# Kernel tuning notes

Measured on AMD Instinct MI355X. Metric: run time of the kernel, lower is better.

## Reference

```python
import jax, jax.numpy as jnp
import numpy as np

LR = 0.001       # ISTA step size (default in _IstaStep)
GAMMA = 0.1      # lambdav sparsity penalty (gamma init kwarg)
N_STEPS = 10     # number of unrolled ISTA iterations


def _soft_threshold(x, t):
    # _proxOp: max(x - t, 0) + min(x + t, 0)
    return jnp.maximum(x - t, 0.0) + jnp.minimum(x + t, 0.0)


def setup_inputs() -> dict:
    key = jax.random.key(0)
    k1, k2 = jax.random.split(key)
    B, I, O = 131072, 128, 256
    inputs = jax.random.normal(k1, (B, I), dtype=jnp.float32)
    # glorot_uniform for W of shape (output_dim, input_dim)
    scale = float(np.sqrt(6.0 / (O + I)))
    W = jax.random.uniform(k2, (O, I), dtype=jnp.float32, minval=-scale, maxval=scale)
    return {"inputs": inputs, "W": W}


def reference(inputs, W):
    # inputs: [B, I]; W: [O, I]; states x: [B, O]
    B = inputs.shape[0]
    O = W.shape[0]
    x0 = jnp.zeros((B, O), dtype=inputs.dtype)

    def step(x, _):
        recon = x @ W                              # [B, I], linear activation
        # analytic grad of sum((inputs - recon)^2) w.r.t. x (what T.grad computes)
        grad = 2.0 * (recon - inputs) @ W.T        # [B, O]
        new_x = _soft_threshold(x - LR * grad, LR * GAMMA)
        # theano.gradient.disconnected_grad on the new state each step
        new_x = jax.lax.stop_gradient(new_x)
        return new_x, None

    x_final, _ = jax.lax.scan(step, x0, None, length=N_STEPS)
    # return_reconstruction=True -> dot(outs, W)
    return x_final @ W
```

## Files before the change

### kernel.cpp

```cpp
#include <hip/hip_runtime.h>
#include <hip/hip_bf16.h>

typedef __attribute__((ext_vector_type(4))) float  f32x4;
typedef __attribute__((ext_vector_type(16))) float f32x16;
typedef __attribute__((ext_vector_type(8))) short  s16x8;
typedef __attribute__((ext_vector_type(4))) short  s16x4;

#define THR_  1.0e-4f
#define SC_   2.0e-3f

__device__ __forceinline__ unsigned short f2bf(float f) {
  union { __hip_bfloat16 b; unsigned short u; } cv;
  cv.b = __float2bfloat16(f);
  return cv.u;
}
__device__ __forceinline__ float sthr(float v) {
  return v - fmaxf(fminf(v, THR_), -THR_);
}
__device__ __forceinline__ float bflo(unsigned u) {
  return __builtin_bit_cast(float, u << 16);
}
__device__ __forceinline__ float bfhi(unsigned u) {
  return __builtin_bit_cast(float, u & 0xffff0000u);
}

__global__ void sc_prep(const float* __restrict__ W, unsigned short* __restrict__ ws) {
  const int b = blockIdx.x;
  const int l = threadIdx.x;
  const int r = l & 31, h = l >> 5;
  if (b < 128) {
    const int kc = b >> 3, ntg = b & 7;
    const int n = ntg * 32 + r;
    const int k0 = kc * 16 + 8 * h;
    float s[8];
    #pragma unroll
    for (int j = 0; j < 8; ++j) s[j] = 0.0f;
    for (int i = 0; i < 128; ++i) {
      const float wn = W[n * 128 + i];
      #pragma unroll
      for (int j = 0; j < 8; ++j) s[j] += W[(k0 + j) * 128 + i] * wn;
    }
    unsigned short* dst = ws + ((unsigned)b * 64u + l) * 8u;
    #pragma unroll
    for (int j = 0; j < 8; ++j) dst[j] = f2bf(-SC_ * s[j]);
  } else if (b < 192) {
    const int bb = b - 128;
    const int kc = bb >> 3, ntg = bb & 7;
    const int n = ntg * 32 + r;
    const int k0 = kc * 16 + 8 * h;
    unsigned short* dst = ws + 65536u + ((unsigned)bb * 64u + l) * 8u;
    #pragma unroll
    for (int j = 0; j < 8; ++j) dst[j] = f2bf(SC_ * W[n * 128 + k0 + j]);
  } else {
    const int bb = b - 192;
    const int kc = bb >> 2, it = bb & 3;
    const int i = it * 32 + r;
    const int n0 = kc * 16 + 8 * h;
    unsigned short* dst = ws + 98304u + ((unsigned)bb * 64u + l) * 8u;
    #pragma unroll
    for (int j = 0; j < 8; ++j) dst[j] = f2bf(W[(n0 + j) * 128 + i]);
  }
}

__global__ __launch_bounds__(256, 2) void sc_fused(
    const float* __restrict__ inp,
    const unsigned short* __restrict__ wsp,
    float* __restrict__ outp)
{
  __shared__ __align__(16) unsigned char lds[33280];

  const int tid = threadIdx.x;
  const int l = tid & 63;
  const int w = tid >> 6;
  const int h = l >> 5;
  const int r31 = l & 31;
  const long row0 = (long)blockIdx.x * 32;

  const int rB0 = r31 * 520 + h * 16;
  const int rB1 = rB0 + 16640;
  const int wB0 = r31 * 520 + h * 8 + w * 128;
  const int wB1 = wB0 + 16640;

  #pragma unroll
  for (int rep = 0; rep < 4; ++rep) {
    const int flat = rep * 256 + tid;
    const int rr = flat >> 5;
    const int c4 = flat & 31;
    const f32x4 v = *reinterpret_cast<const f32x4*>(inp + (row0 + rr) * 128 + c4 * 4);
    s16x4 p;
    p[0] = (short)f2bf(v[0]); p[1] = (short)f2bf(v[1]);
    p[2] = (short)f2bf(v[2]); p[3] = (short)f2bf(v[3]);
    *reinterpret_cast<s16x4*>(lds + 16640 + rr * 264 + c4 * 8) = p;
  }

  s16x8 gfr[32];
  #pragma unroll
  for (int kc = 0; kc < 8; ++kc)
    #pragma unroll
    for (int nt = 0; nt < 2; ++nt)
      gfr[kc * 2 + nt] = *reinterpret_cast<const s16x8*>(
          wsp + 65536u + ((unsigned)(kc * 8 + w * 2 + nt) * 64u + l) * 8u);

  __syncthreads();

  f32x16 accA[2], accB[2], creg[2];
  #pragma unroll
  for (int nt = 0; nt < 2; ++nt)
    #pragma unroll
    for (int e = 0; e < 16; ++e) { accA[nt][e] = 0.0f; accB[nt][e] = 0.0f; }

  const int ib = 16640 + r31 * 264 + h * 16;
  #pragma unroll
  for (int kc = 0; kc < 4; ++kc) {
    const s16x8 bA = *reinterpret_cast<const s16x8*>(lds + ib + kc * 32);
    const s16x8 bB = *reinterpret_cast<const s16x8*>(lds + ib + (kc + 4) * 32);
    __builtin_amdgcn_s_setprio(1);
    #pragma unroll
    for (int nt = 0; nt < 2; ++nt)
      accA[nt] = __builtin_amdgcn_mfma_f32_32x32x16_bf16(gfr[kc * 2 + nt], bA, accA[nt], 0, 0, 0);
    #pragma unroll
    for (int nt = 0; nt < 2; ++nt)
      accB[nt] = __builtin_amdgcn_mfma_f32_32x32x16_bf16(gfr[(kc + 4) * 2 + nt], bB, accB[nt], 0, 0, 0);
    __builtin_amdgcn_s_setprio(0);
  }

  #pragma unroll
  for (int nt = 0; nt < 2; ++nt)
    #pragma unroll
    for (int q = 0; q < 4; ++q) {
      float f0 = accA[nt][4 * q + 0] + accB[nt][4 * q + 0];
      float f1 = accA[nt][4 * q + 1] + accB[nt][4 * q + 1];
      float f2 = accA[nt][4 * q + 2] + accB[nt][4 * q + 2];
      float f3 = accA[nt][4 * q + 3] + accB[nt][4 * q + 3];
      creg[nt][4 * q + 0] = f0; creg[nt][4 * q + 1] = f1;
      creg[nt][4 * q + 2] = f2; creg[nt][4 * q + 3] = f3;
      f0 = sthr(f0); f1 = sthr(f1); f2 = sthr(f2); f3 = sthr(f3);
      s16x4 p;
      p[0] = (short)f2bf(f0); p[1] = (short)f2bf(f1);
      p[2] = (short)f2bf(f2); p[3] = (short)f2bf(f3);
      *reinterpret_cast<s16x4*>(lds + wB0 + nt * 64 + q * 16) = p;
      accA[nt][4 * q + 0] = f0 + creg[nt][4 * q + 0];
      accA[nt][4 * q + 1] = f1 + creg[nt][4 * q + 1];
      accA[nt][4 * q + 2] = f2 + creg[nt][4 * q + 2];
      accA[nt][4 * q + 3] = f3 + creg[nt][4 * q + 3];
      accB[nt][4 * q + 0] = 0.0f; accB[nt][4 * q + 1] = 0.0f;
      accB[nt][4 * q + 2] = 0.0f; accB[nt][4 * q + 3] = 0.0f;
    }

  #pragma unroll
  for (int kc = 0; kc < 16; ++kc)
    #pragma unroll
    for (int nt = 0; nt < 2; ++nt)
      gfr[kc * 2 + nt] = *reinterpret_cast<const s16x8*>(
          wsp + ((unsigned)(kc * 8 + w * 2 + nt) * 64u + l) * 8u);

  if (((blockIdx.x >> 11) ^ blockIdx.x) & 1) {
    __builtin_amdgcn_s_sleep(15);
    __builtin_amdgcn_s_sleep(4);
  }

  auto STEP = [&](const int rb, const int wb) {
    __syncthreads();
    #pragma unroll
    for (int kc = 0; kc < 8; ++kc) {
      const s16x8 bA = *reinterpret_cast<const s16x8*>(lds + rb + kc * 32);
      const s16x8 bB = *reinterpret_cast<const s16x8*>(lds + rb + (kc + 8) * 32);
      __builtin_amdgcn_s_setprio(1);
      #pragma unroll
      for (int nt = 0; nt < 2; ++nt)
        accA[nt] = __builtin_amdgcn_mfma_f32_32x32x16_bf16(gfr[kc * 2 + nt], bA, accA[nt], 0, 0, 0);
      #pragma unroll
      for (int nt = 0; nt < 2; ++nt)
        accB[nt] = __builtin_amdgcn_mfma_f32_32x32x16_bf16(gfr[(kc + 8) * 2 + nt], bB, accB[nt], 0, 0, 0);
      __builtin_amdgcn_s_setprio(0);
    }
    #pragma unroll
    for (int nt = 0; nt < 2; ++nt)
      #pragma unroll
      for (int q = 0; q < 4; ++q) {
        float f0 = sthr(accA[nt][4 * q + 0] + accB[nt][4 * q + 0]);
        float f1 = sthr(accA[nt][4 * q + 1] + accB[nt][4 * q + 1]);
        float f2 = sthr(accA[nt][4 * q + 2] + accB[nt][4 * q + 2]);
        float f3 = sthr(accA[nt][4 * q + 3] + accB[nt][4 * q + 3]);
        s16x4 p;
        p[0] = (short)f2bf(f0); p[1] = (short)f2bf(f1);
        p[2] = (short)f2bf(f2); p[3] = (short)f2bf(f3);
        *reinterpret_cast<s16x4*>(lds + wb + nt * 64 + q * 16) = p;
        accA[nt][4 * q + 0] = f0 + creg[nt][4 * q + 0];
        accA[nt][4 * q + 1] = f1 + creg[nt][4 * q + 1];
        accA[nt][4 * q + 2] = f2 + creg[nt][4 * q + 2];
        accA[nt][4 * q + 3] = f3 + creg[nt][4 * q + 3];
        accB[nt][4 * q + 0] = 0.0f; accB[nt][4 * q + 1] = 0.0f;
        accB[nt][4 * q + 2] = 0.0f; accB[nt][4 * q + 3] = 0.0f;
      }
  };

  #pragma unroll 1
  for (int p = 0; p < 4; ++p) {
    STEP(rB0, wB1);
    STEP(rB1, wB0);
  }
  STEP(rB0, wB1);

  __syncthreads();
  #pragma unroll
  for (int kc = 0; kc < 16; ++kc)
    gfr[kc] = *reinterpret_cast<const s16x8*>(
        wsp + 98304u + ((unsigned)(kc * 4 + w) * 64u + l) * 8u);
  f32x16 oA, oB;
  #pragma unroll
  for (int e = 0; e < 16; ++e) { oA[e] = 0.0f; oB[e] = 0.0f; }
  #pragma unroll
  for (int kc = 0; kc < 8; ++kc) {
    const s16x8 bA = *reinterpret_cast<const s16x8*>(lds + rB1 + kc * 32);
    const s16x8 bB = *reinterpret_cast<const s16x8*>(lds + rB1 + (kc + 8) * 32);
    __builtin_amdgcn_s_setprio(1);
    oA = __builtin_amdgcn_mfma_f32_32x32x16_bf16(gfr[kc], bA, oA, 0, 0, 0);
    oB = __builtin_amdgcn_mfma_f32_32x32x16_bf16(gfr[kc + 8], bB, oB, 0, 0, 0);
    __builtin_amdgcn_s_setprio(0);
  }
  const int ob = r31 * 520 + h * 16 + w * 128;
  #pragma unroll
  for (int q = 0; q < 4; ++q) {
    f32x4 p;
    p[0] = oA[4 * q + 0] + oB[4 * q + 0]; p[1] = oA[4 * q + 1] + oB[4 * q + 1];
    p[2] = oA[4 * q + 2] + oB[4 * q + 2]; p[3] = oA[4 * q + 3] + oB[4 * q + 3];
    *reinterpret_cast<f32x4*>(lds + ob + q * 32) = p;
  }
  __syncthreads();
  #pragma unroll
  for (int rep = 0; rep < 4; ++rep) {
    const int flat = rep * 256 + tid;
    const int rr = flat >> 5;
    const int c4 = flat & 31;
    const f32x4 v = *reinterpret_cast<const f32x4*>(lds + rr * 520 + c4 * 16);
    *reinterpret_cast<f32x4*>(outp + (row0 + rr) * 128 + c4 * 4) = v;
  }
}

extern "C" void kernel_launch(void* const* d_in, const int* in_sizes, int n_in,
                              void* d_out, int out_size, void* d_ws, size_t ws_size,
                              hipStream_t stream) {
  const float* inp = (const float*)d_in[0];
  const float* W   = (const float*)d_in[1];
  unsigned short* ws = (unsigned short*)d_ws;
  float* outp = (float*)d_out;
  const int B = in_sizes[0] / 128;
  sc_prep<<<256, 64, 0, stream>>>(W, ws);
  sc_fused<<<B / 32, 256, 0, stream>>>(inp, ws, outp);
}
```

Baseline: 180.6 us.

## Pack constant term as bf16, prefetch LDS operands, drop staggered sleep

The per-row constant term (creg, 32 floats) is now stored as 16 packed bf16 pairs, which cuts register pressure. The LDS B-operand loads in the step loop are software-pipelined two iterations ahead, and setprio is hoisted out of the loop. The block-parity s_sleep stagger is removed. Storing the constant term in bf16 reduces its precision, and the extra prefetch registers partly offset the savings.

```diff
diff --git a/kernel.cpp b/kernel.cpp
--- a/kernel.cpp
+++ b/kernel.cpp
@@ -103,7 +103,7 @@
 
   __syncthreads();
 
-  f32x16 accA[2], accB[2], creg[2];
+  f32x16 accA[2], accB[2];
   #pragma unroll
   for (int nt = 0; nt < 2; ++nt)
     #pragma unroll
@@ -124,25 +124,30 @@
     __builtin_amdgcn_s_setprio(0);
   }
 
+  unsigned cp[16];
   #pragma unroll
   for (int nt = 0; nt < 2; ++nt)
     #pragma unroll
+    for (int j = 0; j < 8; ++j) {
+      const float e0 = accA[nt][2 * j + 0] + accB[nt][2 * j + 0];
+      const float e1 = accA[nt][2 * j + 1] + accB[nt][2 * j + 1];
+      cp[nt * 8 + j] = (unsigned)f2bf(e0) | ((unsigned)f2bf(e1) << 16);
+    }
+  #pragma unroll
+  for (int nt = 0; nt < 2; ++nt)
+    #pragma unroll
     for (int q = 0; q < 4; ++q) {
-      float f0 = accA[nt][4 * q + 0] + accB[nt][4 * q + 0];
-      float f1 = accA[nt][4 * q + 1] + accB[nt][4 * q + 1];
-      float f2 = accA[nt][4 * q + 2] + accB[nt][4 * q + 2];
-      float f3 = accA[nt][4 * q + 3] + accB[nt][4 * q + 3];
-      creg[nt][4 * q + 0] = f0; creg[nt][4 * q + 1] = f1;
-      creg[nt][4 * q + 2] = f2; creg[nt][4 * q + 3] = f3;
-      f0 = sthr(f0); f1 = sthr(f1); f2 = sthr(f2); f3 = sthr(f3);
+      const unsigned pa = cp[nt * 8 + q * 2], pb = cp[nt * 8 + q * 2 + 1];
+      float f0 = sthr(accA[nt][4 * q + 0] + accB[nt][4 * q + 0]);
+      float f1 = sthr(accA[nt][4 * q + 1] + accB[nt][4 * q + 1]);
+      float f2 = sthr(accA[nt][4 * q + 2] + accB[nt][4 * q + 2]);
+      float f3 = sthr(accA[nt][4 * q + 3] + accB[nt][4 * q + 3]);
       s16x4 p;
       p[0] = (short)f2bf(f0); p[1] = (short)f2bf(f1);
       p[2] = (short)f2bf(f2); p[3] = (short)f2bf(f3);
       *reinterpret_cast<s16x4*>(lds + wB0 + nt * 64 + q * 16) = p;
-      accA[nt][4 * q + 0] = f0 + creg[nt][4 * q + 0];
-      accA[nt][4 * q + 1] = f1 + creg[nt][4 * q + 1];
-      accA[nt][4 * q + 2] = f2 + creg[nt][4 * q + 2];
-      accA[nt][4 * q + 3] = f3 + creg[nt][4 * q + 3];
+      accA[nt][4 * q + 0] = f0 + bflo(pa); accA[nt][4 * q + 1] = f1 + bfhi(pa);
+      accA[nt][4 * q + 2] = f2 + bflo(pb); accA[nt][4 * q + 3] = f3 + bfhi(pb);
       accB[nt][4 * q + 0] = 0.0f; accB[nt][4 * q + 1] = 0.0f;
       accB[nt][4 * q + 2] = 0.0f; accB[nt][4 * q + 3] = 0.0f;
     }
@@ -154,30 +159,32 @@
       gfr[kc * 2 + nt] = *reinterpret_cast<const s16x8*>(
           wsp + ((unsigned)(kc * 8 + w * 2 + nt) * 64u + l) * 8u);
 
-  if (((blockIdx.x >> 11) ^ blockIdx.x) & 1) {
-    __builtin_amdgcn_s_sleep(15);
-    __builtin_amdgcn_s_sleep(4);
-  }
-
   auto STEP = [&](const int rb, const int wb) {
     __syncthreads();
+    s16x8 a0 = *reinterpret_cast<const s16x8*>(lds + rb + 0 * 32);
+    s16x8 b0 = *reinterpret_cast<const s16x8*>(lds + rb + 8 * 32);
+    s16x8 a1 = *reinterpret_cast<const s16x8*>(lds + rb + 1 * 32);
+    s16x8 b1 = *reinterpret_cast<const s16x8*>(lds + rb + 9 * 32);
+    __builtin_amdgcn_s_setprio(1);
     #pragma unroll
     for (int kc = 0; kc < 8; ++kc) {
-      const s16x8 bA = *reinterpret_cast<const s16x8*>(lds + rb + kc * 32);
-      const s16x8 bB = *reinterpret_cast<const s16x8*>(lds + rb + (kc + 8) * 32);
-      __builtin_amdgcn_s_setprio(1);
-      #pragma unroll
-      for (int nt = 0; nt < 2; ++nt)
-        accA[nt] = __builtin_amdgcn_mfma_f32_32x32x16_bf16(gfr[kc * 2 + nt], bA, accA[nt], 0, 0, 0);
-      #pragma unroll
-      for (int nt = 0; nt < 2; ++nt)
-        accB[nt] = __builtin_amdgcn_mfma_f32_32x32x16_bf16(gfr[(kc + 8) * 2 + nt], bB, accB[nt], 0, 0, 0);
-      __builtin_amdgcn_s_setprio(0);
-    }
+      s16x8 a2 = a1, b2 = b1;
+      if (kc < 6) {
+        a2 = *reinterpret_cast<const s16x8*>(lds + rb + (kc + 2) * 32);
+        b2 = *reinterpret_cast<const s16x8*>(lds + rb + (kc + 10) * 32);
+      }
+      accA[0] = __builtin_amdgcn_mfma_f32_32x32x16_bf16(gfr[kc * 2 + 0], a0, accA[0], 0, 0, 0);
+      accA[1] = __builtin_amdgcn_mfma_f32_32x32x16_bf16(gfr[kc * 2 + 1], a0, accA[1], 0, 0, 0);
+      accB[0] = __builtin_amdgcn_mfma_f32_32x32x16_bf16(gfr[(kc + 8) * 2 + 0], b0, accB[0], 0, 0, 0);
+      accB[1] = __builtin_amdgcn_mfma_f32_32x32x16_bf16(gfr[(kc + 8) * 2 + 1], b0, accB[1], 0, 0, 0);
+      a0 = a1; b0 = b1; a1 = a2; b1 = b2;
+    }
+    __builtin_amdgcn_s_setprio(0);
     #pragma unroll
     for (int nt = 0; nt < 2; ++nt)
       #pragma unroll
       for (int q = 0; q < 4; ++q) {
+        const unsigned pa = cp[nt * 8 + q * 2], pb = cp[nt * 8 + q * 2 + 1];
         float f0 = sthr(accA[nt][4 * q + 0] + accB[nt][4 * q + 0]);
         float f1 = sthr(accA[nt][4 * q + 1] + accB[nt][4 * q + 1]);
         float f2 = sthr(accA[nt][4 * q + 2] + accB[nt][4 * q + 2]);
@@ -186,10 +193,8 @@
         p[0] = (short)f2bf(f0); p[1] = (short)f2bf(f1);
         p[2] = (short)f2bf(f2); p[3] = (short)f2bf(f3);
         *reinterpret_cast<s16x4*>(lds + wb + nt * 64 + q * 16) = p;
-        accA[nt][4 * q + 0] = f0 + creg[nt][4 * q + 0];
-        accA[nt][4 * q + 1] = f1 + creg[nt][4 * q + 1];
-        accA[nt][4 * q + 2] = f2 + creg[nt][4 * q + 2];
-        accA[nt][4 * q + 3] = f3 + creg[nt][4 * q + 3];
+        accA[nt][4 * q + 0] = f0 + bflo(pa); accA[nt][4 * q + 1] = f1 + bfhi(pa);
+        accA[nt][4 * q + 2] = f2 + bflo(pb); accA[nt][4 * q + 3] = f3 + bfhi(pb);
         accB[nt][4 * q + 0] = 0.0f; accB[nt][4 * q + 1] = 0.0f;
         accB[nt][4 * q + 2] = 0.0f; accB[nt][4 * q + 3] = 0.0f;
       }
```

After: 176.6 us. -2.2%, faster.
